# Kernel tuning notes

Measured on AMD Instinct MI355X. Metric: run time of the kernel, lower is better.

## Reference

```python
import jax, jax.numpy as jnp
import numpy as np

K_SIZE = 3
SCALE = 4
PADDING = K_SIZE // 2


def setup_inputs() -> dict:
    key = jax.random.key(0)
    k1, k2, k3, k4 = jax.random.split(key, 4)
    B, C, H, W = 8, 3, 1024, 1024
    ho, wo = H // SCALE, W // SCALE
    img = jax.random.normal(k1, (B, C, H, W), dtype=jnp.float32)
    kernels = jax.random.uniform(k2, (B, K_SIZE * K_SIZE, ho, wo), dtype=jnp.float32)
    offsets_h = jax.random.normal(k3, (B, K_SIZE * K_SIZE, ho, wo), dtype=jnp.float32)
    offsets_v = jax.random.normal(k4, (B, K_SIZE * K_SIZE, ho, wo), dtype=jnp.float32)
    offset_unit = jnp.full((1,), 4.0, dtype=jnp.float32)
    return {"img": img, "kernels": kernels, "offsets_h": offsets_h,
            "offsets_v": offsets_v, "offset_unit": offset_unit}


def _adaptive_downsample(img, kernels, offsets_h, offsets_v, offset_unit):
    # img: [B,C,H,W]; kernels/offsets: [B,k^2,ho,wo]; offset_unit: [1]
    B, C, H, W = img.shape
    ho, wo = kernels.shape[2], kernels.shape[3]
    # reflection pad as in nn.ReflectionPad2d(padding)
    imgp = jnp.pad(img, ((0, 0), (0, 0), (PADDING, PADDING), (PADDING, PADDING)), mode="reflect")
    Hp, Wp = imgp.shape[2], imgp.shape[3]

    k = jnp.arange(K_SIZE)
    ky = jnp.repeat(k, K_SIZE).astype(jnp.float32)  # [k^2] row index of kernel tap
    kx = jnp.tile(k, K_SIZE).astype(jnp.float32)    # [k^2] col index of kernel tap

    # output-pixel centers in original image coords; +PADDING shift into padded
    # coords cancels the -PADDING tap centering, so padded sample position is
    # center + k (k in 0..k_size-1).
    cy = (jnp.arange(ho, dtype=jnp.float32) + 0.5) * SCALE - 0.5  # [ho]
    cx = (jnp.arange(wo, dtype=jnp.float32) + 0.5) * SCALE - 0.5  # [wo]

    ou = offset_unit.reshape(())
    # sample positions in padded image, shape [B, k^2, ho, wo]
    p_y = cy[None, None, :, None] + ky[None, :, None, None] + offsets_v * ou
    p_x = cx[None, None, None, :] + kx[None, :, None, None] + offsets_h * ou

    y0f = jnp.floor(p_y)
    x0f = jnp.floor(p_x)
    beta = p_y - y0f   # vertical bilinear weight
    alpha = p_x - x0f  # horizontal bilinear weight

    y0 = jnp.clip(y0f.astype(jnp.int32), 0, Hp - 1)
    y1 = jnp.clip(y0 + 1, 0, Hp - 1)
    x0 = jnp.clip(x0f.astype(jnp.int32), 0, Wp - 1)
    x1 = jnp.clip(x0 + 1, 0, Wp - 1)

    def gather(yi, xi):
        # imgp: [B,C,Hp,Wp]; yi/xi: [B,k^2,ho,wo] -> [B,C,k^2,ho,wo]
        return jax.vmap(lambda im, y, x: im[:, y, x])(imgp, yi, xi)

    v00 = gather(y0, x0)
    v01 = gather(y0, x1)
    v10 = gather(y1, x0)
    v11 = gather(y1, x1)

    a = alpha[:, None]  # [B,1,k^2,ho,wo]
    b_ = beta[:, None]
    val = ((1 - a) * (1 - b_) * v00 + a * (1 - b_) * v01 +
           (1 - a) * b_ * v10 + a * b_ * v11)  # [B,C,k^2,ho,wo]

    # per-pixel learned kernel weighted sum over the k^2 taps
    out = jnp.einsum("bckhw,bkhw->bchw", val, kernels)
    return out


def reference(img, kernels, offsets_h, offsets_v, offset_unit):
    return _adaptive_downsample(img, kernels, offsets_h, offsets_v, offset_unit)
```

## Files before the change

kernel.cpp:

```cpp
#include <hip/hip_runtime.h>
#include <cstdint>

namespace {
constexpr int B = 8, C = 3, H = 1024, W = 1024;
constexpr int HO = 256, WO = 256, K2 = 9;
constexpr int HP = H + 2, WP = W + 2;
constexpr int HW = H * W, HOWO = HO * WO;

constexpr int TW = 32, TH = 16;
constexpr int NTX = WO / TW;
constexpr int NTY = HO / TH;
constexpr int NT  = NTX * NTY;
constexpr int OF = 12;
constexpr int WINW = 4 * TW + 2 * OF;
constexpr int WINH = 4 * TH + 2 * OF;
constexpr int WPX  = WINW * WINH;
constexpr int CPR  = WINW / 4;
constexpr int CHPP = CPR * WINH;
constexpr size_t LDS_BYTES = (size_t)WPX * 12;

__device__ __forceinline__ int reflect_src(int p, int n) {
    int s = p - 1;
    s = (s < 0) ? -s : s;
    s = (s >= n) ? (2 * n - 2 - s) : s;
    return s;
}

__device__ __forceinline__ void dma16(const float* g, float* l) {
    __builtin_amdgcn_global_load_lds(
        (const __attribute__((address_space(1))) unsigned int*)g,
        (__attribute__((address_space(3))) unsigned int*)l,
        16, 0, 0);
}

__global__ __launch_bounds__(512) void ds_dma(
    const float* __restrict__ img,
    const float* __restrict__ kern,
    const float* __restrict__ offh,
    const float* __restrict__ offv,
    const float* __restrict__ ou_p,
    float* __restrict__ out) {
    extern __shared__ __align__(16) float smem[];
    float* __restrict__ win0 = smem;
    float* __restrict__ win1 = smem + WPX;
    float* __restrict__ win2 = smem + 2 * WPX;

    const int b   = blockIdx.x & 7;
    const int t   = blockIdx.x >> 3;
    const int tid = threadIdx.x;
    const int w0  = (t & (NTX - 1)) * TW;
    const int h0  = (t >> 3) * TH;
    const int X0  = 4 * w0 - (OF - 1);
    const int Y0  = 4 * h0 - (OF - 1);

    const float* __restrict__ p0 = img + (size_t)b * (C * HW);
    const float* __restrict__ p1 = p0 + HW;
    const float* __restrict__ p2 = p1 + HW;

    const int lw = tid & (TW - 1);
    const int lh = tid >> 5;
    const int h = h0 + lh, w = w0 + lw;
    const int pb = (b * K2) * HOWO + h * WO + w;
    float kv[K2], vv[K2], hh[K2];
#pragma unroll
    for (int k = 0; k < K2; ++k) {
        kv[k] = kern[pb + k * HOWO];
        vv[k] = offv[pb + k * HOWO];
        hh[k] = offh[pb + k * HOWO];
    }
    const float ou = ou_p[0];

    for (int i = tid; i < CHPP; i += 512) {
        int yy = i / CPR;
        int xc = i - yy * CPR;
        int Yp = min(max(Y0 + yy, 0), HP - 1);
        int sy = reflect_src(Yp, H);
        int gx = X0 - 1 + 4 * xc;
        gx = min(max(gx, 0), W - 4);
        const size_t si = (size_t)sy * W + gx;
        const int lbase = (i & ~63) * 4;
        dma16(p0 + si, win0 + lbase);
        dma16(p1 + si, win1 + lbase);
        dma16(p2 + si, win2 + lbase);
    }
    __syncthreads();

    const bool ledge = (X0 - 1 < 0);
    const bool redge = (X0 - 1 + 4 * (CPR - 1) > W - 4);
    if (ledge | redge) {
        const int xbase = ledge ? 0 : (WINW - 12);
        for (int i = tid; i < 12 * WINH; i += 512) {
            int r = i / 12, cc = i - r * 12;
            int xx = xbase + cc;
            int Yp = min(max(Y0 + r, 0), HP - 1);
            int sy = reflect_src(Yp, H);
            int Xp = min(max(X0 + xx, 0), WP - 1);
            int sx = reflect_src(Xp, W);
            size_t si = (size_t)sy * W + sx;
            int wi = r * WINW + xx;
            win0[wi] = p0[si];
            win1[wi] = p1[si];
            win2[wi] = p2[si];
        }
        __syncthreads();
    }

    const float cy = (h + 0.5f) * 4.0f - 0.5f;
    const float cx = (w + 0.5f) * 4.0f - 0.5f;
    float acc0 = 0.f, acc1 = 0.f, acc2 = 0.f;

#pragma unroll
    for (int k = 0; k < K2; ++k) {
        float py = cy + (float)(k / 3) + vv[k] * ou;
        float px = cx + (float)(k % 3) + hh[k] * ou;

        float y0f = floorf(py), x0f = floorf(px);
        float bb = py - y0f;
        float aa = px - x0f;

        int y0 = min(max((int)y0f, 0), HP - 1);
        int x0 = min(max((int)x0f, 0), WP - 1);
        int y1 = min(y0 + 1, HP - 1);
        int x1 = min(x0 + 1, WP - 1);

        float v00x, v00y, v00z, v01x, v01y, v01z;
        float v10x, v10y, v10z, v11x, v11y, v11z;

        bool inw = (y0 >= Y0) & (y1 <= Y0 + WINH - 1) &
                   (x0 >= X0) & (x1 <= X0 + WINW - 1);
        if (__builtin_expect(inw, 1)) {
            int i00 = (y0 - Y0) * WINW + (x0 - X0);
            int i10 = i00 + (y1 - y0) * WINW;
            bool dx = (x1 > x0);
            float a00 = win0[i00], a01 = win0[i00 + 1];
            float a10 = win0[i10], a11 = win0[i10 + 1];
            float b00 = win1[i00], b01 = win1[i00 + 1];
            float b10 = win1[i10], b11 = win1[i10 + 1];
            float c00 = win2[i00], c01 = win2[i00 + 1];
            float c10 = win2[i10], c11 = win2[i10 + 1];
            v00x = a00; v01x = dx ? a01 : a00;
            v10x = a10; v11x = dx ? a11 : a10;
            v00y = b00; v01y = dx ? b01 : b00;
            v10y = b10; v11y = dx ? b11 : b10;
            v00z = c00; v01z = dx ? c01 : c00;
            v10z = c10; v11z = dx ? c11 : c10;
        } else {
            int sy0 = reflect_src(y0, H), sy1 = reflect_src(y1, H);
            int sx0 = reflect_src(x0, W), sx1 = reflect_src(x1, W);
            size_t i0 = (size_t)sy0 * W + sx0, i1 = (size_t)sy0 * W + sx1;
            size_t i2 = (size_t)sy1 * W + sx0, i3 = (size_t)sy1 * W + sx1;
            v00x = p0[i0]; v01x = p0[i1]; v10x = p0[i2]; v11x = p0[i3];
            v00y = p1[i0]; v01y = p1[i1]; v10y = p1[i2]; v11y = p1[i3];
            v00z = p2[i0]; v01z = p2[i1]; v10z = p2[i2]; v11z = p2[i3];
        }

        float tx_, tu_;
        tx_ = v00x + aa * (v01x - v00x);
        tu_ = v10x + aa * (v11x - v10x);
        acc0 += kv[k] * (tx_ + bb * (tu_ - tx_));
        tx_ = v00y + aa * (v01y - v00y);
        tu_ = v10y + aa * (v11y - v10y);
        acc1 += kv[k] * (tx_ + bb * (tu_ - tx_));
        tx_ = v00z + aa * (v01z - v00z);
        tu_ = v10z + aa * (v11z - v10z);
        acc2 += kv[k] * (tx_ + bb * (tu_ - tx_));
    }

    size_t obase = ((size_t)b * C) * (size_t)HOWO + (size_t)h * WO + w;
    out[obase] = acc0;
    out[obase + (size_t)HOWO] = acc1;
    out[obase + (size_t)(2 * HOWO)] = acc2;
}
}

extern "C" void kernel_launch(void* const* d_in, const int* in_sizes, int n_in,
                              void* d_out, int out_size, void* d_ws, size_t ws_size,
                              hipStream_t stream) {
    const float* img  = (const float*)d_in[0];
    const float* kern = (const float*)d_in[1];
    const float* offh = (const float*)d_in[2];
    const float* offv = (const float*)d_in[3];
    const float* ou   = (const float*)d_in[4];
    float* out = (float*)d_out;

    static bool attr_set = false;
    if (!attr_set) {
        hipFuncSetAttribute(reinterpret_cast<const void*>(&ds_dma),
                            hipFuncAttributeMaxDynamicSharedMemorySize,
                            (int)LDS_BYTES);
        attr_set = true;
    }

    hipLaunchKernelGGL(ds_dma, dim3(B * NT), dim3(512), LDS_BYTES, stream,
                       img, kern, offh, offv, ou, out);
}
```

Measured before the change: 209.5 us.

## Precompute sample indices during DMA and batch LDS loads before blending

Sample positions, bilinear weights and LDS indices are now computed for all nine taps while the window DMA is still in flight, so that math overlaps the load. After the barrier, all 108 LDS reads are issued in one batch and then blended, and out-of-window taps are handled in a separate wave-uniform fallback pass. The launch bounds ask for two blocks per CU. The batched loads raise register pressure, which may conflict with the occupancy target and cause spills.

```diff
diff --git a/kernel.cpp b/kernel.cpp
--- a/kernel.cpp
+++ b/kernel.cpp
@@ -17,7 +17,7 @@
 constexpr int WPX  = WINW * WINH;
 constexpr int CPR  = WINW / 4;
 constexpr int CHPP = CPR * WINH;
-constexpr size_t LDS_BYTES = (size_t)WPX * 12;
+constexpr size_t LDS_BYTES = (size_t)WPX * 12 + 16;
 
 __device__ __forceinline__ int reflect_src(int p, int n) {
     int s = p - 1;
@@ -33,7 +33,7 @@
         16, 0, 0);
 }
 
-__global__ __launch_bounds__(512) void ds_dma(
+__global__ __launch_bounds__(512, 2) void ds_batch(
     const float* __restrict__ img,
     const float* __restrict__ kern,
     const float* __restrict__ offh,
@@ -82,6 +82,34 @@
         dma16(p0 + si, win0 + lbase);
         dma16(p1 + si, win1 + lbase);
         dma16(p2 + si, win2 + lbase);
+    }
+
+    const float cy = (h + 0.5f) * 4.0f - 0.5f;
+    const float cx = (w + 0.5f) * 4.0f - 0.5f;
+    int   i00c[K2], i10c[K2];
+    bool  dxs[K2];
+    float aav[K2], bbv[K2], kve[K2];
+    unsigned oow = 0;
+#pragma unroll
+    for (int k = 0; k < K2; ++k) {
+        float py = cy + (float)(k / 3) + vv[k] * ou;
+        float px = cx + (float)(k % 3) + hh[k] * ou;
+        float y0f = floorf(py), x0f = floorf(px);
+        bbv[k] = py - y0f;
+        aav[k] = px - x0f;
+        int y0 = min(max((int)y0f, 0), HP - 1);
+        int x0 = min(max((int)x0f, 0), WP - 1);
+        int y1 = min(y0 + 1, HP - 1);
+        int x1 = min(x0 + 1, WP - 1);
+        bool inw = (y0 >= Y0) & (y1 <= Y0 + WINH - 1) &
+                   (x0 >= X0) & (x1 <= X0 + WINW - 1);
+        int i00 = (y0 - Y0) * WINW + (x0 - X0);
+        int i10 = i00 + (y1 - y0) * WINW;
+        i00c[k] = inw ? i00 : 0;
+        i10c[k] = inw ? i10 : 0;
+        dxs[k]  = inw & (x1 > x0);
+        kve[k]  = inw ? kv[k] : 0.f;
+        oow |= (inw ? 0u : 1u) << k;
     }
     __syncthreads();
 
@@ -105,65 +133,73 @@
         __syncthreads();
     }
 
-    const float cy = (h + 0.5f) * 4.0f - 0.5f;
-    const float cx = (w + 0.5f) * 4.0f - 0.5f;
+    float a00[K2], a01[K2], a10[K2], a11[K2];
+    float b00[K2], b01[K2], b10[K2], b11[K2];
+    float c00[K2], c01[K2], c10[K2], c11[K2];
+#pragma unroll
+    for (int k = 0; k < K2; ++k) {
+        int i0 = i00c[k], i1 = i10c[k];
+        a00[k] = win0[i0]; a01[k] = win0[i0 + 1];
+        a10[k] = win0[i1]; a11[k] = win0[i1 + 1];
+        b00[k] = win1[i0]; b01[k] = win1[i0 + 1];
+        b10[k] = win1[i1]; b11[k] = win1[i1 + 1];
+        c00[k] = win2[i0]; c01[k] = win2[i0 + 1];
+        c10[k] = win2[i1]; c11[k] = win2[i1 + 1];
+    }
+
     float acc0 = 0.f, acc1 = 0.f, acc2 = 0.f;
-
-#pragma unroll
-    for (int k = 0; k < K2; ++k) {
-        float py = cy + (float)(k / 3) + vv[k] * ou;
-        float px = cx + (float)(k % 3) + hh[k] * ou;
-
-        float y0f = floorf(py), x0f = floorf(px);
-        float bb = py - y0f;
-        float aa = px - x0f;
-
-        int y0 = min(max((int)y0f, 0), HP - 1);
-        int x0 = min(max((int)x0f, 0), WP - 1);
-        int y1 = min(y0 + 1, HP - 1);
-        int x1 = min(x0 + 1, WP - 1);
-
-        float v00x, v00y, v00z, v01x, v01y, v01z;
-        float v10x, v10y, v10z, v11x, v11y, v11z;
-
-        bool inw = (y0 >= Y0) & (y1 <= Y0 + WINH - 1) &
-                   (x0 >= X0) & (x1 <= X0 + WINW - 1);
-        if (__builtin_expect(inw, 1)) {
-            int i00 = (y0 - Y0) * WINW + (x0 - X0);
-            int i10 = i00 + (y1 - y0) * WINW;
-            bool dx = (x1 > x0);
-            float a00 = win0[i00], a01 = win0[i00 + 1];
-            float a10 = win0[i10], a11 = win0[i10 + 1];
-            float b00 = win1[i00], b01 = win1[i00 + 1];
-            float b10 = win1[i10], b11 = win1[i10 + 1];
-            float c00 = win2[i00], c01 = win2[i00 + 1];
-            float c10 = win2[i10], c11 = win2[i10 + 1];
-            v00x = a00; v01x = dx ? a01 : a00;
-            v10x = a10; v11x = dx ? a11 : a10;
-            v00y = b00; v01y = dx ? b01 : b00;
-            v10y = b10; v11y = dx ? b11 : b10;
-            v00z = c00; v01z = dx ? c01 : c00;
-            v10z = c10; v11z = dx ? c11 : c10;
-        } else {
-            int sy0 = reflect_src(y0, H), sy1 = reflect_src(y1, H);
-            int sx0 = reflect_src(x0, W), sx1 = reflect_src(x1, W);
-            size_t i0 = (size_t)sy0 * W + sx0, i1 = (size_t)sy0 * W + sx1;
-            size_t i2 = (size_t)sy1 * W + sx0, i3 = (size_t)sy1 * W + sx1;
-            v00x = p0[i0]; v01x = p0[i1]; v10x = p0[i2]; v11x = p0[i3];
-            v00y = p1[i0]; v01y = p1[i1]; v10y = p1[i2]; v11y = p1[i3];
-            v00z = p2[i0]; v01z = p2[i1]; v10z = p2[i2]; v11z = p2[i3];
+#pragma unroll
+    for (int k = 0; k < K2; ++k) {
+        float aa = aav[k], bb = bbv[k], kw = kve[k];
+        float s01 = dxs[k] ? a01[k] : a00[k];
+        float s11 = dxs[k] ? a11[k] : a10[k];
+        float t01 = dxs[k] ? b01[k] : b00[k];
+        float t11 = dxs[k] ? b11[k] : b10[k];
+        float u01 = dxs[k] ? c01[k] : c00[k];
+        float u11 = dxs[k] ? c11[k] : c10[k];
+        float tx_, tu_;
+        tx_ = a00[k] + aa * (s01 - a00[k]);
+        tu_ = a10[k] + aa * (s11 - a10[k]);
+        acc0 += kw * (tx_ + bb * (tu_ - tx_));
+        tx_ = b00[k] + aa * (t01 - b00[k]);
+        tu_ = b10[k] + aa * (t11 - b10[k]);
+        acc1 += kw * (tx_ + bb * (tu_ - tx_));
+        tx_ = c00[k] + aa * (u01 - c00[k]);
+        tu_ = c10[k] + aa * (u11 - c10[k]);
+        acc2 += kw * (tx_ + bb * (tu_ - tx_));
+    }
+
+    if (__builtin_expect(__any(oow != 0), 0)) {
+#pragma unroll
+        for (int k = 0; k < K2; ++k) {
+            bool bad = (oow >> k) & 1u;
+            if (__any(bad)) {
+                if (bad) {
+                    float py = cy + (float)(k / 3) + vv[k] * ou;
+                    float px = cx + (float)(k % 3) + hh[k] * ou;
+                    float y0f = floorf(py), x0f = floorf(px);
+                    float bb = py - y0f, aa = px - x0f;
+                    int y0 = min(max((int)y0f, 0), HP - 1);
+                    int x0 = min(max((int)x0f, 0), WP - 1);
+                    int y1 = min(y0 + 1, HP - 1);
+                    int x1 = min(x0 + 1, WP - 1);
+                    int sy0 = reflect_src(y0, H), sy1 = reflect_src(y1, H);
+                    int sx0 = reflect_src(x0, W), sx1 = reflect_src(x1, W);
+                    size_t j0 = (size_t)sy0 * W + sx0, j1 = (size_t)sy0 * W + sx1;
+                    size_t j2 = (size_t)sy1 * W + sx0, j3 = (size_t)sy1 * W + sx1;
+                    float tx_, tu_;
+                    tx_ = p0[j0] + aa * (p0[j1] - p0[j0]);
+                    tu_ = p0[j2] + aa * (p0[j3] - p0[j2]);
+                    acc0 += kv[k] * (tx_ + bb * (tu_ - tx_));
+                    tx_ = p1[j0] + aa * (p1[j1] - p1[j0]);
+                    tu_ = p1[j2] + aa * (p1[j3] - p1[j2]);
+                    acc1 += kv[k] * (tx_ + bb * (tu_ - tx_));
+                    tx_ = p2[j0] + aa * (p2[j1] - p2[j0]);
+                    tu_ = p2[j2] + aa * (p2[j3] - p2[j2]);
+                    acc2 += kv[k] * (tx_ + bb * (tu_ - tx_));
+                }
+            }
         }
-
-        float tx_, tu_;
-        tx_ = v00x + aa * (v01x - v00x);
-        tu_ = v10x + aa * (v11x - v10x);
-        acc0 += kv[k] * (tx_ + bb * (tu_ - tx_));
-        tx_ = v00y + aa * (v01y - v00y);
-        tu_ = v10y + aa * (v11y - v10y);
-        acc1 += kv[k] * (tx_ + bb * (tu_ - tx_));
-        tx_ = v00z + aa * (v01z - v00z);
-        tu_ = v10z + aa * (v11z - v10z);
-        acc2 += kv[k] * (tx_ + bb * (tu_ - tx_));
     }
 
     size_t obase = ((size_t)b * C) * (size_t)HOWO + (size_t)h * WO + w;
@@ -185,12 +221,12 @@
 
     static bool attr_set = false;
     if (!attr_set) {
-        hipFuncSetAttribute(reinterpret_cast<const void*>(&ds_dma),
+        hipFuncSetAttribute(reinterpret_cast<const void*>(&ds_batch),
                             hipFuncAttributeMaxDynamicSharedMemorySize,
                             (int)LDS_BYTES);
         attr_set = true;
     }
 
-    hipLaunchKernelGGL(ds_dma, dim3(B * NT), dim3(512), LDS_BYTES, stream,
+    hipLaunchKernelGGL(ds_batch, dim3(B * NT), dim3(512), LDS_BYTES, stream,
                        img, kern, offh, offv, ou, out);
 }
```

New measurement: 209.4 us. Within noise of the previous version (-0.1%).
